# Optimization experiments

Hardware: AMD Instinct MI355X
Metric: run time of the kernel (lower is better)

## Reference

```python
import jax, jax.numpy as jnp
import numpy as np
from jax import lax

H = 16          # heads
K1, K2 = 3, 3   # kernel_size
LN_EPS = 1e-5


def _ln(x, g, b):
    m = jnp.mean(x, axis=-1, keepdims=True)
    v = jnp.mean(jnp.square(x - m), axis=-1, keepdims=True)
    return (x - m) * lax.rsqrt(v + LN_EPS) * g + b


def _gelu(x):
    return jax.nn.gelu(x, approximate=False)  # torch nn.GELU default (erf)


def setup_inputs() -> dict:
    key = jax.random.key(0)
    B, T, D, Th = 4, 1024, 1024, 256
    C = 2 * D  # context_dim
    ks = jax.random.split(key, 16)

    def w(k, shape):
        fan_in = shape[0]
        return (jax.random.normal(k, shape, jnp.float32) / np.sqrt(fan_in)).astype(jnp.float32)

    inp = {
        'x': jax.random.normal(ks[0], (B, T, D), jnp.float32),
        'historical_data': jax.random.normal(ks[1], (B, Th, D), jnp.float32),
        'Wq': w(ks[2], (D, D)),
        'Wk': w(ks[3], (D, D)),
        'Wv': w(ks[4], (D, D)),
        'hist_W': w(ks[5], (D, C)), 'hist_b': jnp.zeros((C,), jnp.float32),
        'hist_ln_g': jnp.ones((C,), jnp.float32), 'hist_ln_b': jnp.zeros((C,), jnp.float32),
        'ctx_W1': w(ks[6], (C, C // 4)), 'ctx_b1': jnp.zeros((C // 4,), jnp.float32),
        'ctx_W2': w(ks[7], (C // 4, 1)), 'ctx_b2': jnp.zeros((1,), jnp.float32),
        'kg_W1': w(ks[8], (C, D)), 'kg_b1': jnp.zeros((D,), jnp.float32),
        'kg_ln_g': jnp.ones((D,), jnp.float32), 'kg_ln_b': jnp.zeros((D,), jnp.float32),
        'kg_W2': w(ks[9], (D, H * K1 * K2)), 'kg_b2': jnp.zeros((H * K1 * K2,), jnp.float32),
        'proj_W': w(ks[10], (D, D)), 'proj_b': jnp.zeros((D,), jnp.float32),
        'causal_mask': jnp.triu(jnp.ones((T, T), bool), k=1),  # True = masked
    }
    return inp


def reference(x, historical_data, Wq, Wk, Wv, hist_W, hist_b, hist_ln_g, hist_ln_b,
              ctx_W1, ctx_b1, ctx_W2, ctx_b2, kg_W1, kg_b1, kg_ln_g, kg_ln_b,
              kg_W2, kg_b2, proj_W, proj_b, causal_mask):
    B, T, D = x.shape
    hd = D // H
    scale = hd ** -0.5

    # qkv projections (no bias), split heads -> [B, H, T, hd]
    q = (x @ Wq).reshape(B, T, H, hd).transpose(0, 2, 1, 3)
    k = (x @ Wk).reshape(B, T, H, hd).transpose(0, 2, 1, 3)
    v = (x @ Wv).reshape(B, T, H, hd).transpose(0, 2, 1, 3)

    attn = jnp.einsum('bhqd,bhkd->bhqk', q, k) * scale  # [B,H,T,T]

    # --- causal context from history ---
    eh = _gelu(_ln(historical_data @ hist_W + hist_b, hist_ln_g, hist_ln_b))  # [B,Th,C]
    aw = _gelu(eh @ ctx_W1 + ctx_b1) @ ctx_W2 + ctx_b2                        # [B,Th,1]
    aw = jax.nn.softmax(aw, axis=1)
    cc = jnp.sum(eh * aw, axis=1)                                             # [B,C]

    # --- per-(batch,head) 3x3 kernels ---
    kp = _gelu(_ln(cc @ kg_W1 + kg_b1, kg_ln_g, kg_ln_b)) @ kg_W2 + kg_b2     # [B,H*9]
    kernels = jax.nn.softmax(kp.reshape(B, H, K1 * K2), axis=-1)
    kernels = kernels.reshape(B * H, 1, K1, K2)

    # zero masked scores, then mix neighbors via grouped conv2d (cross-correlation)
    mask = causal_mask[None, None]  # [1,1,T,T]
    attn0 = jnp.where(mask, 0.0, attn).reshape(1, B * H, T, T)
    attn = lax.conv_general_dilated(
        attn0, kernels, window_strides=(1, 1),
        padding=((K1 // 2, K1 // 2), (K2 // 2, K2 // 2)),
        feature_group_count=B * H,
        dimension_numbers=('NCHW', 'OIHW', 'NCHW'),
    ).reshape(B, H, T, T)

    attn = jnp.where(mask, -jnp.inf, attn)
    p = jax.nn.softmax(attn, axis=-1)
    out = jnp.einsum('bhqk,bhkd->bhqd', p, v)           # [B,H,T,hd]
    out = out.transpose(0, 2, 1, 3).reshape(B, T, D)
    return out @ proj_W + proj_b
```

## Files before the change

kernel.cpp:

```cpp
#include <hip/hip_runtime.h>
#include <hip/hip_bf16.h>
#include <math.h>

#define DEV static __device__ __forceinline__

typedef __attribute__((ext_vector_type(4))) float f32x4;
typedef __attribute__((ext_vector_type(8))) __bf16 bf16x8;
typedef __attribute__((ext_vector_type(8))) short s16x8;
typedef __attribute__((ext_vector_type(2))) _Float16 h16x2;

DEV float b2f(short v){ unsigned u = ((unsigned)(unsigned short)v) << 16; float f; __builtin_memcpy(&f, &u, 4); return f; }
DEV short f2b(float f){ unsigned u; __builtin_memcpy(&u, &f, 4); unsigned r = (u + 0x7fffu + ((u >> 16) & 1u)) >> 16; return (short)r; }
DEV short f2h(float f){ _Float16 h = (_Float16)f; short s; __builtin_memcpy(&s, &h, 2); return s; }
DEV h16x2 u2h2(unsigned u){ h16x2 h; __builtin_memcpy(&h, &u, 4); return h; }
DEV float gelu_f(float v){ return 0.5f * v * (1.0f + erff(v * 0.70710678118654752f)); }

DEV void gload16(const void* g, void* l) {
  __builtin_amdgcn_global_load_lds((const __attribute__((address_space(1))) unsigned int*)g,
                                   (__attribute__((address_space(3))) unsigned int*)l, 16, 0, 0);
}

DEV void xy_swz(int& bx, int& by, int nx, int ny) {
  int lin = by * nx + bx;
  int q = (nx * ny) >> 3;
  int l2 = (lin & 7) * q + (lin >> 3);
  bx = l2 % nx; by = l2 / nx;
}

__global__ __launch_bounds__(256) void k_cast_all(const float* __restrict__ x, const float* __restrict__ hist,
                                                  short* __restrict__ xb, short* __restrict__ histb,
                                                  short* __restrict__ q, short* __restrict__ kk){
  int bid = blockIdx.x;
  if (bid >= 2560) {
    int idx = (bid - 2560) * 256 + threadIdx.x;
    int bh = idx >> 5, c = idx & 31;
    int which = c >> 3, chunk = c & 7;
    short* base = (which < 2) ? q : kk;
    size_t off = (size_t)bh * 1026 * 64 + ((which & 1) ? (size_t)1025 * 64 : 0) + chunk * 8;
    s16x8 zz = {};
    *(s16x8*)&base[off] = zz;
    return;
  }
  const float* in; short* out; int i;
  if (bid < 2048) { in = x; out = xb; i = (bid * 256 + threadIdx.x) * 8; }
  else            { in = hist; out = histb; i = ((bid - 2048) * 256 + threadIdx.x) * 8; }
  f32x4 a = *(const f32x4*)&in[i];
  f32x4 b = *(const f32x4*)&in[i + 4];
  s16x8 o;
  o[0]=f2b(a[0]); o[1]=f2b(a[1]); o[2]=f2b(a[2]); o[3]=f2b(a[3]);
  o[4]=f2b(b[0]); o[5]=f2b(b[1]); o[6]=f2b(b[2]); o[7]=f2b(b[3]);
  *(s16x8*)&out[i] = o;
}

DEV void tcast_tile(const float* __restrict__ W, short* __restrict__ Wt, int K, int N, int tx, int ty){
  __shared__ float tile[32][33];
  int nb = tx * 32, kb = ty * 32;
  int tid = threadIdx.x;
  int c = tid & 31, r0 = tid >> 5;
  #pragma unroll
  for (int r = r0; r < 32; r += 8) tile[r][c] = W[(size_t)(kb + r) * N + nb + c];
  __syncthreads();
  #pragma unroll
  for (int r = r0; r < 32; r += 8) Wt[(size_t)(nb + r) * K + kb + c] = f2b(tile[c][r]);
}
__global__ __launch_bounds__(256) void k_tcast_all(const float* __restrict__ Wq, const float* __restrict__ Wk,
                                                   const float* __restrict__ Wv, const float* __restrict__ projW,
                                                   const float* __restrict__ histW, const float* __restrict__ ctxW1,
                                                   short* __restrict__ wqkvt, short* __restrict__ wptb,
                                                   short* __restrict__ whtb, short* __restrict__ wc1tb){
  int bid = blockIdx.x;
  const float* W; short* Wt; int K, N, tx, ty;
  if (bid < 4096) {
    int seg = bid >> 10, t = bid & 1023;
    tx = t & 31; ty = t >> 5; K = 1024; N = 1024;
    if      (seg == 0) { W = Wq;    Wt = wqkvt; }
    else if (seg == 1) { W = Wk;    Wt = wqkvt + 1024*1024; }
    else if (seg == 2) { W = Wv;    Wt = wqkvt + 2*1024*1024; }
    else               { W = projW; Wt = wptb; }
  } else if (bid < 6144) {
    int t = bid - 4096; tx = t & 63; ty = t >> 6; K = 1024; N = 2048; W = histW; Wt = whtb;
  } else {
    int t = bid - 6144; tx = t & 15; ty = t >> 4; K = 2048; N = 512; W = ctxW1; Wt = wc1tb;
  }
  tcast_tile(W, Wt, K, N, tx, ty);
}

DEV void gemm_core(const short* __restrict__ A, const short* __restrict__ Bt,
                   int Ks, int lda, int ldb, int m0, int n0,
                   short* lA, short* lB, f32x4 acc[4][4])
{
  const int tid = threadIdx.x;
  const int lane = tid & 63;
  const int w = tid >> 6;
  const int wr = (w >> 1) * 64, wc = (w & 1) * 64;
  const int lr = lane & 15, lk = (lane >> 4) * 8;
  for (int kt = 0; kt < Ks; kt += 64) {
    __syncthreads();
    #pragma unroll
    for (int i = 0; i < 4; ++i) {
      int off = i * 2048 + tid * 8;
      int r = off >> 6, c = off & 63;
      gload16(&A[(size_t)(m0 + r) * lda + kt + c], &lA[off]);
      gload16(&Bt[(size_t)(n0 + r) * ldb + kt + c], &lB[off]);
    }
    __syncthreads();
    #pragma unroll
    for (int kk = 0; kk < 64; kk += 32) {
      bf16x8 af[4], bfr[4];
      #pragma unroll
      for (int mi = 0; mi < 4; ++mi) af[mi] = *(bf16x8*)&lA[(wr + mi*16 + lr)*64 + kk + lk];
      #pragma unroll
      for (int ni = 0; ni < 4; ++ni) bfr[ni] = *(bf16x8*)&lB[(wc + ni*16 + lr)*64 + kk + lk];
      #pragma unroll
      for (int mi = 0; mi < 4; ++mi)
        #pragma unroll
        for (int ni = 0; ni < 4; ++ni)
          acc[mi][ni] = __builtin_amdgcn_mfma_f32_16x16x32_bf16(af[mi], bfr[ni], acc[mi][ni], 0, 0, 0);
    }
  }
}

__global__ __launch_bounds__(256) void k_gemm_f32out(const short* __restrict__ A, const short* __restrict__ Bt,
                                                     float* __restrict__ Cout, const float* __restrict__ bias,
                                                     int N, int lda, int Ks, int mode)
{
  __shared__ __align__(16) short lds[2 * 128 * 64];
  f32x4 acc[4][4] = {};
  int bx = blockIdx.x, by = blockIdx.y;
  xy_swz(bx, by, gridDim.x, gridDim.y);
  int m0 = by * 128, n0 = bx * 128;
  int koff = blockIdx.z * Ks;
  gemm_core(A + koff, Bt + koff, Ks, lda, lda, m0, n0, lds, lds + 128*64, acc);
  Cout += (size_t)blockIdx.z * gridDim.y * 128 * N;
  int lane = threadIdx.x & 63, w = threadIdx.x >> 6;
  int wr = (w>>1)*64, wc = (w&1)*64, lr4 = (lane>>4)*4, lc = lane & 15;
  #pragma unroll
  for (int mi = 0; mi < 4; ++mi)
    #pragma unroll
    for (int ni = 0; ni < 4; ++ni)
      #pragma unroll
      for (int r = 0; r < 4; ++r) {
        int row = m0 + wr + mi*16 + lr4 + r;
        int col = n0 + wc + ni*16 + lc;
        float v = acc[mi][ni][r];
        if (mode != 2) v += bias[col];
        if (mode == 1) v = gelu_f(v);
        Cout[(size_t)row * N + col] = v;
      }
}

__global__ __launch_bounds__(256) void k_gemm_qkv(const short* __restrict__ xb, const short* __restrict__ wqkvt,
                                                  short* __restrict__ q, short* __restrict__ kk, short* __restrict__ vt)
{
  __shared__ __align__(16) short lds[128 * 136];
  f32x4 acc[4][4] = {};
  int bx = blockIdx.x, by = blockIdx.y;
  xy_swz(bx, by, gridDim.x, gridDim.y);
  int m0 = by * 128, n0 = bx * 128;
  gemm_core(xb, wqkvt, 1024, 1024, 1024, m0, n0, lds, lds + 128*64, acc);
  int tid = threadIdx.x, lane = tid & 63, w = tid >> 6;
  int wr = (w>>1)*64, wc = (w&1)*64, lr4 = (lane>>4)*4, lc = lane & 15;
  int bb = m0 >> 10, tm0 = m0 & 1023;
  int s = n0 >> 10, dn0 = n0 & 1023;
  __syncthreads();
  if (s < 2) {
    short* dst = (s == 0) ? q : kk;
    #pragma unroll
    for (int mi = 0; mi < 4; ++mi)
      #pragma unroll
      for (int ni = 0; ni < 4; ++ni)
        #pragma unroll
        for (int r = 0; r < 4; ++r)
          lds[(wr + mi*16 + lr4 + r) * 136 + wc + ni*16 + lc] = f2b(acc[mi][ni][r]);
    __syncthreads();
    #pragma unroll
    for (int it = 0; it < 8; ++it) {
      int idx = it * 256 + tid;
      int row = idx >> 4, ch = (idx & 15) * 8;
      int dfull = dn0 + ch;
      *(s16x8*)&dst[((size_t)(bb*16 + (dfull >> 6)) * 1026 + 1 + tm0 + row) * 64 + (dfull & 63)]
          = *(s16x8*)&lds[row * 136 + ch];
    }
  } else {
    #pragma unroll
    for (int mi = 0; mi < 4; ++mi)
      #pragma unroll
      for (int ni = 0; ni < 4; ++ni)
        #pragma unroll
        for (int r = 0; r < 4; ++r)
          lds[(wc + ni*16 + lc) * 136 + wr + mi*16 + lr4 + r] = f2b(acc[mi][ni][r]);
    __syncthreads();
    #pragma unroll
    for (int it = 0; it < 8; ++it) {
      int idx = it * 256 + tid;
      int nl = idx >> 4, mc = (idx & 15) * 8;
      int dfull = dn0 + nl;
      *(s16x8*)&vt[(((size_t)(bb*16 + (dfull >> 6)) * 64 + (dfull & 63)) << 10) + tm0 + mc]
          = *(s16x8*)&lds[nl * 136 + mc];
    }
  }
}

constexpr int ASTR = 132;

DEV void conv_chunk(const short* sS, int g, int c,
                    const h16x2 wp01[3], const h16x2 wp2z[3], float o[8]) {
  #pragma unroll
  for (int dr = 0; dr < 3; ++dr) {
    int base = (g + dr) * ASTR + 8 + c;
    const unsigned* W = (const unsigned*)&sS[base];
    unsigned U0 = W[0], U1 = W[1], U2 = W[2], U3 = W[3];
    unsigned hm1 = (unsigned short)sS[base - 1];
    unsigned hp8 = (unsigned short)sS[base + 8];
    unsigned P0 = hm1 | (U0 << 16);
    unsigned P2 = (U0 >> 16) | (U1 << 16);
    unsigned P4 = (U1 >> 16) | (U2 << 16);
    unsigned P6 = (U2 >> 16) | (U3 << 16);
    unsigned P8 = (U3 >> 16) | (hp8 << 16);
    unsigned P9 = hp8;
    unsigned pr[10] = {P0, U0, P2, U1, P4, U2, P6, U3, P8, P9};
    h16x2 a = wp01[dr], bz = wp2z[dr];
    #pragma unroll
    for (int t = 0; t < 8; ++t) {
      o[t] = __builtin_amdgcn_fdot2(a,  u2h2(pr[t]),     o[t], false);
      o[t] = __builtin_amdgcn_fdot2(bz, u2h2(pr[t + 2]), o[t], false);
    }
  }
}

__global__ __launch_bounds__(256, 4) void k_attn(const short* __restrict__ q, const short* __restrict__ kkg,
                                                 const short* __restrict__ vt, const float* __restrict__ kern,
                                                 short* __restrict__ O)
{
  __shared__ __align__(16) short lK[144 * 64];
  __shared__ __align__(16) short lS[66 * ASTR];

  int bh = blockIdx.y, b = bh >> 4, h = bh & 15;
  int x2 = blockIdx.x;
  int qt2 = ((bh >> 4) & 1) ? 15 - x2 : x2;
  int m0 = qt2 * 64;
  int qtK = qt2 >> 1, odd = qt2 & 1;
  int tid = threadIdx.x;
  int w = tid >> 6, lane = tid & 63;
  int lr = lane & 15, hi = lane >> 4;
  int lk = hi * 8;

  const short* qp = q   + (size_t)bh * 1026 * 64;
  const short* kp = kkg + (size_t)bh * 1026 * 64;

  h16x2 wp01[3], wp2z[3];
  #pragma unroll
  for (int a = 0; a < 3; ++a) {
    wp01[a][0] = (_Float16)kern[bh * 9 + a * 3 + 0];
    wp01[a][1] = (_Float16)kern[bh * 9 + a * 3 + 1];
    wp2z[a][0] = (_Float16)kern[bh * 9 + a * 3 + 2];
    wp2z[a][1] = (_Float16)0.0f;
  }

  bf16x8 qf0, qf1;
  {
    const short* qrow = &qp[(size_t)(m0 + w * 16 + lr) * 64];
    qf0 = *(const bf16x8*)&qrow[lk];
    qf1 = *(const bf16x8*)&qrow[32 + lk];
  }
  bf16x8 qe0, qe1;
  {
    const short* qrow = &qp[(size_t)(m0 + 50 + lr) * 64];
    qe0 = *(const bf16x8*)&qrow[lk];
    qe1 = *(const bf16x8*)&qrow[32 + lk];
  }

  s16x8 zz = {};
  for (int t = tid; t < 14 * 8; t += 256)
    *(s16x8*)&lK[(130 * 8 + t) * 8] = zz;
  for (int t = tid; t < 130 * 8; t += 256) {
    int r = t >> 3;
    gload16(&kp[((size_t)r) * 64 + (((t & 7) ^ (r & 7)) << 3)], &lK[t * 8]);
  }

  f32x4 pacc[4] = {};
  float psum = 0.0f;

  for (int ct = 0; ct <= qtK; ++ct) {
    int n0 = ct * 128;
    if (ct) {
      for (int t = tid; t < 130 * 8; t += 256) {
        int r = t >> 3;
        gload16(&kp[((size_t)(n0 + r)) * 64 + (((t & 7) ^ (r & 7)) << 3)], &lK[t * 8]);
      }
    }
    __syncthreads();

    int ntmax = (ct == qtK) ? (w + 2 + 4 * odd) : 9;
    for (int nt = 0; nt < ntmax; ++nt) {
      int krow = nt * 16 + lr;
      int sw = (krow & 7) << 3;
      bf16x8 bk0 = *(bf16x8*)&lK[krow * 64 + (( hi      << 3) ^ sw)];
      bf16x8 bk1 = *(bf16x8*)&lK[krow * 64 + (((hi + 4) << 3) ^ sw)];
      f32x4 acc = {};
      acc = __builtin_amdgcn_mfma_f32_16x16x32_bf16(qf0, bk0, acc, 0, 0, 0);
      acc = __builtin_amdgcn_mfma_f32_16x16x32_bf16(qf1, bk1, acc, 0, 0, 0);
      int cloc = krow - 1;
      if (cloc <= 128) {
        #pragma unroll
        for (int r = 0; r < 4; ++r) {
          int rl = w * 16 + hi * 4 + r;
          float v = acc[r] * 0.125f;
          if (n0 + cloc > m0 - 1 + rl) v = 0.0f;
          lS[rl * ASTR + 8 + cloc] = f2h(v);
        }
      }
    }
    int ntlim_e = (ct == qtK) ? (4 + 4 * odd) : 8;
    #pragma unroll
    for (int e = 0; e < 3; ++e) {
      int nt = w + 4 * e;
      if (nt > ntlim_e) continue;
      int krow = nt * 16 + lr;
      int sw = (krow & 7) << 3;
      bf16x8 bk0 = *(bf16x8*)&lK[krow * 64 + (( hi      << 3) ^ sw)];
      bf16x8 bk1 = *(bf16x8*)&lK[krow * 64 + (((hi + 4) << 3) ^ sw)];
      f32x4 acc = {};
      acc = __builtin_amdgcn_mfma_f32_16x16x32_bf16(qe0, bk0, acc, 0, 0, 0);
      acc = __builtin_amdgcn_mfma_f32_16x16x32_bf16(qe1, bk1, acc, 0, 0, 0);
      int cloc = krow - 1;
      if (hi == 3 && cloc <= 128) {
        #pragma unroll
        for (int r = 2; r < 4; ++r) {
          int rowt = 12 + r;
          float v = acc[r] * 0.125f;
          if (n0 + cloc > m0 + 49 + rowt) v = 0.0f;
          lS[(50 + rowt) * ASTR + 8 + cloc] = f2h(v);
        }
      }
    }
    __syncthreads();

    int g = w * 16 + lr;
    int glim = (ct == qtK) ? (64 * odd + g) : 127;
    s16x8 pa[4];
    #pragma unroll
    for (int j = 0; j < 4; ++j) {
      int c = hi * 8 + 32 * j;
      bool live = (c <= glim);
      float o[8] = {};
      if (live) conv_chunk(lS, g, c, wp01, wp2z, o);
      s16x8 po;
      #pragma unroll
      for (int t = 0; t < 8; ++t) {
        float e = (live && (c + t <= glim)) ? __expf(o[t]) : 0.0f;
        psum += e;
        po[t] = f2b(e);
      }
      pa[j] = po;
    }

    int kl = 128;
    if (ct == qtK) { kl = ((64 * odd + w * 16 + 16 + 31) >> 5) << 5; if (kl > 128) kl = 128; }
    #pragma unroll
    for (int j = 0; j < 4; ++j) {
      if (j * 32 < kl) {
        bf16x8 af;
        __builtin_memcpy(&af, &pa[j], 16);
        #pragma unroll
        for (int dt = 0; dt < 4; ++dt) {
          bf16x8 bv = *(const bf16x8*)&vt[(((size_t)bh * 64 + dt * 16 + lr) << 10) + n0 + j * 32 + lk];
          pacc[dt] = __builtin_amdgcn_mfma_f32_16x16x32_bf16(af, bv, pacc[dt], 0, 0, 0);
        }
      }
    }
  }

  psum += __shfl_xor(psum, 16);
  psum += __shfl_xor(psum, 32);
  #pragma unroll
  for (int r = 0; r < 4; ++r) {
    float sInvR = 1.0f / __shfl(psum, hi * 4 + r, 64);
    int row = w * 16 + hi * 4 + r;
    #pragma unroll
    for (int dt = 0; dt < 4; ++dt) {
      float ov = pacc[dt][r] * sInvR;
      O[((size_t)(b * 1024 + m0 + row) << 10) + h * 64 + dt * 16 + lr] = f2b(ov);
    }
  }
}

__global__ __launch_bounds__(256) void k_ln_gelu2048(const float* __restrict__ x, const float* __restrict__ cb,
                                                     const float* __restrict__ g, const float* __restrict__ be,
                                                     short* __restrict__ out)
{
  __shared__ float red[8];
  int row = blockIdx.x, tid = threadIdx.x;
  const float* xr0 = x + (size_t)row * 2048;
  const float* xr1 = x + (size_t)(1024 + row) * 2048;
  int c0 = tid * 8;
  f32x4 a  = *(const f32x4*)&xr0[c0];
  f32x4 bb = *(const f32x4*)&xr0[c0 + 4];
  f32x4 a1 = *(const f32x4*)&xr1[c0];
  f32x4 b1 = *(const f32x4*)&xr1[c0 + 4];
  f32x4 cb0 = *(const f32x4*)&cb[c0], cb1 = *(const f32x4*)&cb[c0 + 4];
  a += a1 + cb0; bb += b1 + cb1;
  float s = 0, s2 = 0;
  #pragma unroll
  for (int t = 0; t < 4; ++t) { s += a[t] + bb[t]; s2 += a[t]*a[t] + bb[t]*bb[t]; }
  #pragma unroll
  for (int off = 32; off; off >>= 1) { s += __shfl_xor(s, off); s2 += __shfl_xor(s2, off); }
  if ((tid & 63) == 0) { red[tid >> 6] = s; red[4 + (tid >> 6)] = s2; }
  __syncthreads();
  s  = red[0] + red[1] + red[2] + red[3];
  s2 = red[4] + red[5] + red[6] + red[7];
  float mean = s * (1.0f / 2048.0f);
  float var  = s2 * (1.0f / 2048.0f) - mean * mean;
  float inv  = rsqrtf(var + 1e-5f);
  f32x4 g0 = *(const f32x4*)&g[c0],  g1 = *(const f32x4*)&g[c0 + 4];
  f32x4 e0 = *(const f32x4*)&be[c0], e1 = *(const f32x4*)&be[c0 + 4];
  s16x8 o;
  #pragma unroll
  for (int t = 0; t < 4; ++t) {
    o[t]     = f2b(gelu_f((a[t]  - mean) * inv * g0[t] + e0[t]));
    o[t + 4] = f2b(gelu_f((bb[t] - mean) * inv * g1[t] + e1[t]));
  }
  *(s16x8*)&out[(size_t)row * 2048 + c0] = o;
}

__global__ __launch_bounds__(256) void k_red_gelu(const float* __restrict__ p, const float* __restrict__ b1,
                                                  float* __restrict__ out)
{
  int i = (blockIdx.x * 256 + threadIdx.x) * 4;
  f32x4 s = *(const f32x4*)&p[i];
  #pragma unroll
  for (int z = 1; z < 4; ++z) s += *(const f32x4*)&p[(size_t)z * 524288 + i];
  f32x4 bv = *(const f32x4*)&b1[i & 511];
  f32x4 o;
  #pragma unroll
  for (int t = 0; t < 4; ++t) o[t] = gelu_f(s[t] + bv[t]);
  *(f32x4*)&out[i] = o;
}

__global__ __launch_bounds__(256) void k_aw_logit(const float* __restrict__ t, const float* __restrict__ w2,
                                                  const float* __restrict__ b2, float* __restrict__ logit)
{
  int row = blockIdx.x * 4 + (threadIdx.x >> 6);
  int lane = threadIdx.x & 63;
  float s = 0;
  for (int c = lane; c < 512; c += 64) s += t[(size_t)row * 512 + c] * w2[c];
  #pragma unroll
  for (int off = 32; off; off >>= 1) s += __shfl_xor(s, off);
  if (lane == 0) logit[row] = s + b2[0];
}

__global__ __launch_bounds__(256) void k_softmax_cc(const float* __restrict__ logit, const short* __restrict__ ehb,
                                                    float* __restrict__ cc)
{
  __shared__ float sw[256];
  __shared__ float red[8];
  int b = blockIdx.y, ch = blockIdx.x, tid = threadIdx.x;
  float v = logit[b * 256 + tid];
  float m = v;
  #pragma unroll
  for (int off = 32; off; off >>= 1) m = fmaxf(m, __shfl_xor(m, off));
  if ((tid & 63) == 0) red[tid >> 6] = m;
  __syncthreads();
  float M = fmaxf(fmaxf(red[0], red[1]), fmaxf(red[2], red[3]));
  float e = __expf(v - M);
  float s = e;
  #pragma unroll
  for (int off = 32; off; off >>= 1) s += __shfl_xor(s, off);
  if ((tid & 63) == 0) red[4 + (tid >> 6)] = s;
  __syncthreads();
  float invS = 1.0f / (red[4] + red[5] + red[6] + red[7]);
  sw[tid] = e * invS;
  __syncthreads();
  int c = ch * 256 + tid;
  float a = 0;
  for (int t = 0; t < 256; ++t) a += sw[t] * b2f(ehb[(((size_t)(b * 256 + t)) << 11) + c]);
  cc[(b << 11) + c] = a;
}

__global__ __launch_bounds__(256) void k_kg1p(const float* __restrict__ cc, const float* __restrict__ W1,
                                              float* __restrict__ part)
{
  int d = blockIdx.x * 256 + threadIdx.x;
  int kc = blockIdx.y;
  float s0 = 0, s1 = 0, s2 = 0, s3 = 0;
  for (int k = kc * 64; k < kc * 64 + 64; ++k) {
    float w = W1[(size_t)k * 1024 + d];
    s0 += cc[k] * w; s1 += cc[2048 + k] * w; s2 += cc[4096 + k] * w; s3 += cc[6144 + k] * w;
  }
  part[(size_t)(kc * 4 + 0) * 1024 + d] = s0;
  part[(size_t)(kc * 4 + 1) * 1024 + d] = s1;
  part[(size_t)(kc * 4 + 2) * 1024 + d] = s2;
  part[(size_t)(kc * 4 + 3) * 1024 + d] = s3;
}

__global__ __launch_bounds__(256) void k_kg_mid(const float* __restrict__ part, const float* __restrict__ b1,
                                                const float* __restrict__ g, const float* __restrict__ be,
                                                short* __restrict__ kgh)
{
  __shared__ float red[8];
  int b = blockIdx.x, tid = threadIdx.x;
  float v[4]; float s = 0, s2 = 0;
  #pragma unroll
  for (int qi = 0; qi < 4; ++qi) {
    int d = tid + qi * 256;
    float acc = b1[d];
    for (int kc = 0; kc < 32; ++kc) acc += part[(size_t)(kc * 4 + b) * 1024 + d];
    v[qi] = acc; s += acc; s2 += acc * acc;
  }
  #pragma unroll
  for (int off = 32; off; off >>= 1) { s += __shfl_xor(s, off); s2 += __shfl_xor(s2, off); }
  if ((tid & 63) == 0) { red[tid >> 6] = s; red[4 + (tid >> 6)] = s2; }
  __syncthreads();
  s  = red[0] + red[1] + red[2] + red[3];
  s2 = red[4] + red[5] + red[6] + red[7];
  float mean = s * (1.0f / 1024.0f);
  float var  = s2 * (1.0f / 1024.0f) - mean * mean;
  float inv  = rsqrtf(var + 1e-5f);
  #pragma unroll
  for (int qi = 0; qi < 4; ++qi) {
    int d = tid + qi * 256;
    kgh[b * 1024 + d] = f2b(gelu_f((v[qi] - mean) * inv * g[d] + be[d]));
  }
}

__global__ __launch_bounds__(64) void k_kp2(const short* __restrict__ kgh, const float* __restrict__ W2,
                                            const float* __restrict__ b2, float* __restrict__ kern)
{
  int h = blockIdx.x, b = blockIdx.y, lane = threadIdx.x;
  float kg[16];
  #pragma unroll
  for (int m = 0; m < 16; ++m) kg[m] = b2f(kgh[b * 1024 + lane + m * 64]);
  float dj[9];
  #pragma unroll
  for (int j = 0; j < 9; ++j) {
    float s = 0;
    #pragma unroll
    for (int m = 0; m < 16; ++m) s += kg[m] * W2[(size_t)(lane + m * 64) * 144 + h * 9 + j];
    #pragma unroll
    for (int off = 32; off; off >>= 1) s += __shfl_xor(s, off);
    dj[j] = s + b2[h * 9 + j];
  }
  if (lane == 0) {
    float m = dj[0];
    #pragma unroll
    for (int j = 1; j < 9; ++j) m = fmaxf(m, dj[j]);
    float e[9], s = 0;
    #pragma unroll
    for (int j = 0; j < 9; ++j) { e[j] = __expf(dj[j] - m); s += e[j]; }
    float inv = 1.0f / s;
    #pragma unroll
    for (int j = 0; j < 9; ++j) kern[(b * 16 + h) * 9 + j] = e[j] * inv;
  }
}

__global__ void k_fail(float* out){ out[threadIdx.x] = 1.0e9f; }

extern "C" void kernel_launch(void* const* d_in, const int* in_sizes, int n_in,
                              void* d_out, int out_size, void* d_ws, size_t ws_size,
                              hipStream_t stream) {
  (void)in_sizes; (void)n_in; (void)out_size;
  const float* x       = (const float*)d_in[0];
  const float* hist    = (const float*)d_in[1];
  const float* Wq      = (const float*)d_in[2];
  const float* Wk      = (const float*)d_in[3];
  const float* Wv      = (const float*)d_in[4];
  const float* hist_W  = (const float*)d_in[5];
  const float* hist_b  = (const float*)d_in[6];
  const float* hln_g   = (const float*)d_in[7];
  const float* hln_b   = (const float*)d_in[8];
  const float* ctx_W1  = (const float*)d_in[9];
  const float* ctx_b1  = (const float*)d_in[10];
  const float* ctx_W2  = (const float*)d_in[11];
  const float* ctx_b2  = (const float*)d_in[12];
  const float* kg_W1   = (const float*)d_in[13];
  const float* kg_b1   = (const float*)d_in[14];
  const float* kln_g   = (const float*)d_in[15];
  const float* kln_b   = (const float*)d_in[16];
  const float* kg_W2   = (const float*)d_in[17];
  const float* kg_b2   = (const float*)d_in[18];
  const float* proj_W  = (const float*)d_in[19];
  const float* proj_b  = (const float*)d_in[20];
  float* outp = (float*)d_out;

  char* wsb = (char*)d_ws;
  size_t off = 0;
  auto nxt = [&](size_t bytes) { void* p = wsb + off; off += (bytes + 255) & ~(size_t)255; return p; };

  short* xb     = (short*)nxt((size_t)4096*1024*2);
  short* wqkvt  = (short*)nxt((size_t)3*1024*1024*2);
  short* qb     = (short*)nxt((size_t)64*1026*64*2);
  short* kb     = (short*)nxt((size_t)64*1026*64*2);
  short* vtb    = (short*)nxt((size_t)64*64*1024*2);
  short* Ob     = (short*)nxt((size_t)4096*1024*2);
  short* histb  = (short*)nxt((size_t)1024*1024*2);
  short* whtb   = (short*)nxt((size_t)2048*1024*2);
  float* ehpreP = (float*)nxt((size_t)2*1024*2048*4);
  short* ehb    = (short*)nxt((size_t)1024*2048*2);
  short* wc1tb  = (short*)nxt((size_t)512*2048*2);
  float* ctxP   = (float*)nxt((size_t)4*1024*512*4);
  float* tbuf   = (float*)nxt((size_t)1024*512*4);
  float* logit  = (float*)nxt((size_t)1024*4);
  float* ccb    = (float*)nxt((size_t)4*2048*4);
  float* kgpart = (float*)nxt((size_t)128*1024*4);
  short* kghb   = (short*)nxt((size_t)4*1024*2);
  float* kernb  = (float*)nxt((size_t)64*9*4);
  short* wptb   = (short*)nxt((size_t)1024*1024*2);

  if (ws_size < off) { k_fail<<<1, 64, 0, stream>>>(outp); return; }

  k_cast_all<<<2568, 256, 0, stream>>>(x, hist, xb, histb, qb, kb);
  k_tcast_all<<<7168, 256, 0, stream>>>(Wq, Wk, Wv, proj_W, hist_W, ctx_W1, wqkvt, wptb, whtb, wc1tb);

  k_gemm_f32out<<<dim3(16, 8, 2), 256, 0, stream>>>(histb, whtb, ehpreP, nullptr, 2048, 1024, 512, 2);
  k_ln_gelu2048<<<1024, 256, 0, stream>>>(ehpreP, hist_b, hln_g, hln_b, ehb);
  k_gemm_f32out<<<dim3(4, 8, 4), 256, 0, stream>>>(ehb, wc1tb, ctxP, nullptr, 512, 2048, 512, 2);
  k_red_gelu<<<512, 256, 0, stream>>>(ctxP, ctx_b1, tbuf);
  k_aw_logit<<<256, 256, 0, stream>>>(tbuf, ctx_W2, ctx_b2, logit);
  k_softmax_cc<<<dim3(8, 4), 256, 0, stream>>>(logit, ehb, ccb);
  k_kg1p<<<dim3(4, 32), 256, 0, stream>>>(ccb, kg_W1, kgpart);
  k_kg_mid<<<4, 256, 0, stream>>>(kgpart, kg_b1, kln_g, kln_b, kghb);
  k_kp2<<<dim3(16, 4), 64, 0, stream>>>(kghb, kg_W2, kg_b2, kernb);

  k_gemm_qkv<<<dim3(24, 32), 256, 0, stream>>>(xb, wqkvt, qb, kb, vtb);
  k_attn<<<dim3(16, 64), 256, 0, stream>>>(qb, kb, vtb, kernb, Ob);
  k_gemm_f32out<<<dim3(8, 32, 1), 256, 0, stream>>>(Ob, wptb, outp, proj_b, 1024, 1024, 1024, 0);
}
```

Before: 263.2 us.

## Prefetch next K tile into registers to overlap loads with score compute

Replaces the synchronous global-to-LDS K tile loads with register prefetching. The next tile is loaded into registers while the current tile's QK scores are computed, then written to LDS after the barrier, during the conv/softmax phase. This hides global load latency behind MFMA work, at the cost of extra VGPRs (five 16-byte vectors per thread) and possibly lower occupancy.

```diff
diff --git a/kernel.cpp b/kernel.cpp
--- a/kernel.cpp
+++ b/kernel.cpp
@@ -271,25 +271,40 @@
   }
 
   s16x8 zz = {};
+  s16x8 kr0, kr1, kr2, kr3, kr4 = zz;
+  {
+    int t0 = tid;
+    #define KSRC(t) (&kp[((size_t)((t) >> 3)) * 64 + ((((t) & 7) ^ (((t) >> 3) & 7)) << 3)])
+    kr0 = *(const s16x8*)KSRC(t0);
+    kr1 = *(const s16x8*)KSRC(t0 + 256);
+    kr2 = *(const s16x8*)KSRC(t0 + 512);
+    kr3 = *(const s16x8*)KSRC(t0 + 768);
+    if (tid < 16) kr4 = *(const s16x8*)KSRC(t0 + 1024);
+  }
   for (int t = tid; t < 14 * 8; t += 256)
     *(s16x8*)&lK[(130 * 8 + t) * 8] = zz;
-  for (int t = tid; t < 130 * 8; t += 256) {
-    int r = t >> 3;
-    gload16(&kp[((size_t)r) * 64 + (((t & 7) ^ (r & 7)) << 3)], &lK[t * 8]);
-  }
+  *(s16x8*)&lK[tid * 8]          = kr0;
+  *(s16x8*)&lK[(tid + 256) * 8]  = kr1;
+  *(s16x8*)&lK[(tid + 512) * 8]  = kr2;
+  *(s16x8*)&lK[(tid + 768) * 8]  = kr3;
+  if (tid < 16) *(s16x8*)&lK[(tid + 1024) * 8] = kr4;
 
   f32x4 pacc[4] = {};
   float psum = 0.0f;
 
   for (int ct = 0; ct <= qtK; ++ct) {
     int n0 = ct * 128;
-    if (ct) {
-      for (int t = tid; t < 130 * 8; t += 256) {
-        int r = t >> 3;
-        gload16(&kp[((size_t)(n0 + r)) * 64 + (((t & 7) ^ (r & 7)) << 3)], &lK[t * 8]);
-      }
-    }
     __syncthreads();
+
+    if (ct < qtK) {
+      const short* kpn = kp + (size_t)(n0 + 128) * 64;
+      #define KSRC2(t) (&kpn[((size_t)((t) >> 3)) * 64 + ((((t) & 7) ^ (((t) >> 3) & 7)) << 3)])
+      kr0 = *(const s16x8*)KSRC2(tid);
+      kr1 = *(const s16x8*)KSRC2(tid + 256);
+      kr2 = *(const s16x8*)KSRC2(tid + 512);
+      kr3 = *(const s16x8*)KSRC2(tid + 768);
+      if (tid < 16) kr4 = *(const s16x8*)KSRC2(tid + 1024);
+    }
 
     int ntmax = (ct == qtK) ? (w + 2 + 4 * odd) : 9;
     for (int nt = 0; nt < ntmax; ++nt) {
@@ -335,6 +350,14 @@
       }
     }
     __syncthreads();
+
+    if (ct < qtK) {
+      *(s16x8*)&lK[tid * 8]          = kr0;
+      *(s16x8*)&lK[(tid + 256) * 8]  = kr1;
+      *(s16x8*)&lK[(tid + 512) * 8]  = kr2;
+      *(s16x8*)&lK[(tid + 768) * 8]  = kr3;
+      if (tid < 16) *(s16x8*)&lK[(tid + 1024) * 8] = kr4;
+    }
 
     int g = w * 16 + lr;
     int glim = (ct == qtK) ? (64 * odd + g) : 127;
```

Result: slower. 285.6 us (+8.5%).
